# Kernel tuning notes

Measured on AMD Instinct MI355X. Metric: run time of the kernel, lower is better.

Reference implementation:

```python
import jax, jax.numpy as jnp
import numpy as np
from jax import lax

N, D, K = 8192, 1024, 80
M = 2048            # pre-NMS candidate budget (jit-static stand-in for nonzero())
TOPK = 100
IMG_H, IMG_W = 800.0, 1216.0
BW = (10.0, 10.0, 5.0, 5.0)            # Box2BoxTransform weights
SCALE_CLAMP = float(np.log(1000.0 / 16.0))
SCORE_T, NMS_T = 0.05, 0.5
MAX_COORD = max(IMG_H, IMG_W) + 1.0    # class offset for batched NMS


def setup_inputs() -> dict:
    key = jax.random.key(0)
    ks = jax.random.split(key, 5)
    x = jax.random.normal(ks[0], (N, D), jnp.float32)
    cls_w = jax.random.normal(ks[1], (D, K + 1), jnp.float32) * 0.1
    cls_b = jnp.zeros((K + 1,), jnp.float32)
    bbox_w = jax.random.normal(ks[2], (D, K * 4), jnp.float32) * 0.001
    bbox_b = jnp.zeros((K * 4,), jnp.float32)
    xy = jax.random.uniform(ks[3], (N, 2)) * jnp.array([IMG_W * 0.8, IMG_H * 0.8])
    wh = jax.random.uniform(ks[4], (N, 2)) * jnp.array([IMG_W * 0.2, IMG_H * 0.2]) + 8.0
    proposals = jnp.concatenate([xy, xy + wh], axis=1).astype(jnp.float32)  # [N,4] xyxy
    return {"x": x, "cls_w": cls_w, "cls_b": cls_b,
            "bbox_w": bbox_w, "bbox_b": bbox_b, "proposals": proposals}


def _apply_deltas(deltas, boxes):
    # deltas [N,K,4], boxes [N,4] xyxy -> decoded [N,K,4]
    w = boxes[:, 2] - boxes[:, 0]
    h = boxes[:, 3] - boxes[:, 1]
    cx = boxes[:, 0] + 0.5 * w
    cy = boxes[:, 1] + 0.5 * h
    dx = deltas[..., 0] / BW[0]
    dy = deltas[..., 1] / BW[1]
    dw = jnp.minimum(deltas[..., 2] / BW[2], SCALE_CLAMP)
    dh = jnp.minimum(deltas[..., 3] / BW[3], SCALE_CLAMP)
    pcx = dx * w[:, None] + cx[:, None]
    pcy = dy * h[:, None] + cy[:, None]
    pw = jnp.exp(dw) * w[:, None]
    ph = jnp.exp(dh) * h[:, None]
    return jnp.stack([pcx - 0.5 * pw, pcy - 0.5 * ph,
                      pcx + 0.5 * pw, pcy + 0.5 * ph], axis=-1)


def _clip(b):
    x1 = jnp.clip(b[..., 0], 0.0, IMG_W)
    y1 = jnp.clip(b[..., 1], 0.0, IMG_H)
    x2 = jnp.clip(b[..., 2], 0.0, IMG_W)
    y2 = jnp.clip(b[..., 3], 0.0, IMG_H)
    return jnp.stack([x1, y1, x2, y2], axis=-1)


def _pairwise_iou(b):  # [M,4] -> [M,M]
    x1 = jnp.maximum(b[:, None, 0], b[None, :, 0])
    y1 = jnp.maximum(b[:, None, 1], b[None, :, 1])
    x2 = jnp.minimum(b[:, None, 2], b[None, :, 2])
    y2 = jnp.minimum(b[:, None, 3], b[None, :, 3])
    inter = jnp.maximum(x2 - x1, 0.0) * jnp.maximum(y2 - y1, 0.0)
    area = (b[:, 2] - b[:, 0]) * (b[:, 3] - b[:, 1])
    union = area[:, None] + area[None, :] - inter
    return inter / jnp.maximum(union, 1e-9)


def _pipeline(x, cls_w, cls_b, bbox_w, bbox_b, proposals):
    probs = jax.nn.softmax(x @ cls_w + cls_b, axis=-1)[:, :K]   # drop bg col
    deltas = (x @ bbox_w + bbox_b).reshape(N, K, 4)
    boxes = _clip(_apply_deltas(deltas, proposals))             # [N,K,4]

    flat = probs.reshape(-1)                                    # [N*K]
    cand = jnp.where(flat > SCORE_T, flat, -1.0)
    top_scores, top_idx = lax.top_k(cand, M)                    # sorted desc
    prop_idx = top_idx // K
    cls_idx = top_idx % K
    cand_boxes = boxes[prop_idx, cls_idx]                       # [M,4]
    valid = top_scores > SCORE_T

    # batched NMS via per-class coordinate offsets
    off = cls_idx.astype(cand_boxes.dtype)[:, None] * MAX_COORD
    iou = _pairwise_iou(cand_boxes + off)
    idxs = jnp.arange(M)

    def body(i, sup):
        alive = jnp.logical_and(~sup[i], valid[i])
        return sup | (alive & (iou[i] > NMS_T) & (idxs > i))

    sup = lax.fori_loop(0, M, body, jnp.zeros((M,), bool))
    keep = valid & ~sup

    kept_scores = jnp.where(keep, top_scores, -1.0)
    fscores, fidx = lax.top_k(kept_scores, TOPK)
    fboxes = cand_boxes[fidx]
    fcls = cls_idx[fidx]
    fvalid = keep[fidx]
    return fboxes, fscores, fcls, fvalid


def reference(x, cls_w, cls_b, bbox_w, bbox_b, proposals):
    return _pipeline(x, cls_w, cls_b, bbox_w, bbox_b, proposals)
```

## Files before the change

### kernel.cpp

```cpp
#include <hip/hip_runtime.h>
#include <math.h>

typedef unsigned long long u64;
typedef unsigned int u32;

#define N_ROWS 8192
#define DIM 1024
#define KCLS 80
#define KC1 81
#define MCAND 2048
#define TOPK_ 100
#define CMAX 65536
#define ECAP 4096
#define ROWS_CAP 4096
#define EROWS 3
#define EKS 4
#define EKL (DIM / EKS)
#define FRPB 8
#define NSPLIT 16
#define NBINS 8192
#define BIN_BASE 125440
#define LCAP 1024
#define SCORE_T 0.05
#define NMS_T 0.5f
#define MAX_COORD_F 1217.0f
#define SCALE_CLAMP_F 4.135166556742356f
#define IMG_W_F 1216.0f
#define IMG_H_F 800.0f

#define GBM 32
#define GBK 64
#define PSTR 96
#define WFRAG (32 * 6 * 64 * 8)

typedef __attribute__((ext_vector_type(8))) short bf16x8;
typedef __attribute__((ext_vector_type(4))) float f32x4;

__device__ __forceinline__ int score_bin_f(float p) {
  u32 bits = __float_as_uint(p);
  int b = (int)(bits >> 13) - BIN_BASE;
  return b < 0 ? 0 : (b > NBINS - 1 ? NBINS - 1 : b);
}

__device__ __forceinline__ u64 readlane64(u64 v, int l) {
  u32 lo = __builtin_amdgcn_readlane((u32)v, l);
  u32 hi = __builtin_amdgcn_readlane((u32)(v >> 32), l);
  return ((u64)hi << 32) | (u64)lo;
}

__device__ __forceinline__ ushort f32_bf16(float f) {
  u32 b = __float_as_uint(f);
  b += 0x7FFFu + ((b >> 16) & 1u);
  return (ushort)(b >> 16);
}

__global__ __launch_bounds__(256) void k_prep(
    int* counter, int* ecount, int* rowcnt, int* hist, int* cnt,
    u32* rowflag, double* selS, u32* selI,
    const float4* __restrict__ bw4, float4* __restrict__ wT4,
    const float* __restrict__ w, ushort* __restrict__ whiF,
    ushort* __restrict__ wloF)
{
  int t = blockIdx.x * 256 + threadIdx.x;
  if (t == 0) { *counter = 0; *ecount = 0; *rowcnt = 0; }
  if (t < NBINS) hist[t] = 0;
  if (t < N_ROWS) rowflag[t] = 0;
  if (t < ECAP) cnt[t] = 0;
  if (t < MCAND) { selS[t] = -1.0; selI[t] = 0u; }
  if (t < KCLS * DIM) {
    int k = t / KCLS;
    int cls = t - k * KCLS;
    wT4[(size_t)cls * DIM + k] = bw4[t];
  }
  if (t < WFRAG) {
    int j = t & 7;
    int l = (t >> 3) & 63;
    int sf = t >> 9;
    int f = sf % 6;
    int s = sf / 6;
    int k = s * 32 + (l >> 4) * 8 + j;
    int c = f * 16 + (l & 15);
    float v = (c < KC1) ? w[(size_t)k * KC1 + c] : 0.0f;
    ushort hi = f32_bf16(v);
    float hf = __uint_as_float((u32)hi << 16);
    whiF[t] = hi;
    wloF[t] = f32_bf16(v - hf);
  }
}

__global__ __launch_bounds__(256) void k_gemm_sm(
    const float* __restrict__ x, const ushort* __restrict__ whiF,
    const ushort* __restrict__ wloF, const float* __restrict__ bias,
    float* __restrict__ scf, u32* __restrict__ cid,
    int* __restrict__ counter, int* __restrict__ hist)
{
  __shared__ __align__(16) char smem[33792];
  __shared__ float lgs[GBM * PSTR];
  __shared__ int lcnt, gbase;

  ushort (*xhi)[72] = (ushort(*)[72])(smem);
  ushort (*xlo)[72] = (ushort(*)[72])(smem + 4608);
  uint4* bhi = (uint4*)(smem + 9216);
  uint4* blo = (uint4*)(smem + 21504);
  u32* lhist = (u32*)(smem);
  float* lscf = (float*)(smem + 16384);
  u32* lcid = (u32*)(smem + 20480);
  float (*red)[32] = (float(*)[32])(smem + 24576);
  float* rowM = (float*)(smem + 26624);
  float* rowS = (float*)(smem + 26752);

  const int tid = threadIdx.x;
  const int rb = blockIdx.x * GBM;
  const int l = tid & 63;
  const int wv = tid >> 6;
  const int rh = wv & 1;
  const int ch = wv >> 1;

  if (tid == 0) lcnt = 0;

  f32x4 acc0 = {0.f, 0.f, 0.f, 0.f};
  f32x4 acc1 = {0.f, 0.f, 0.f, 0.f};
  f32x4 acc2 = {0.f, 0.f, 0.f, 0.f};

  const int srow = tid >> 3;
  const int skq = (tid & 7) * 8;
  const float* xsrc = x + (size_t)(rb + srow) * DIM + skq;

  const int ar = rh * 16 + (l & 15);
  const int ak = (l >> 4) * 8;
  const int bbase = (ch * 3) * 64 + l;

  for (int kt = 0; kt < DIM; kt += GBK) {
    float4 xv0 = *(const float4*)(xsrc + kt);
    float4 xv1 = *(const float4*)(xsrc + kt + 4);
    const uint4* bh = (const uint4*)whiF + (size_t)(kt >> 5) * 384;
    const uint4* bl = (const uint4*)wloF + (size_t)(kt >> 5) * 384;
    uint4 h0 = bh[tid], h1 = bh[tid + 256], h2 = bh[tid + 512];
    uint4 g0 = bl[tid], g1 = bl[tid + 256], g2 = bl[tid + 512];

    __syncthreads();

    {
      float vv[8] = {xv0.x, xv0.y, xv0.z, xv0.w, xv1.x, xv1.y, xv1.z, xv1.w};
      u32 hw[4], lw[4];
#pragma unroll
      for (int q = 0; q < 4; ++q) {
        ushort ha = f32_bf16(vv[2 * q]);
        ushort hb = f32_bf16(vv[2 * q + 1]);
        ushort la = f32_bf16(vv[2 * q] - __uint_as_float((u32)ha << 16));
        ushort lb = f32_bf16(vv[2 * q + 1] - __uint_as_float((u32)hb << 16));
        hw[q] = (u32)ha | ((u32)hb << 16);
        lw[q] = (u32)la | ((u32)lb << 16);
      }
      *(uint4*)&xhi[srow][skq] = make_uint4(hw[0], hw[1], hw[2], hw[3]);
      *(uint4*)&xlo[srow][skq] = make_uint4(lw[0], lw[1], lw[2], lw[3]);
      bhi[tid] = h0; bhi[tid + 256] = h1; bhi[tid + 512] = h2;
      blo[tid] = g0; blo[tid + 256] = g1; blo[tid + 512] = g2;
    }
    __syncthreads();

#pragma unroll
    for (int ks = 0; ks < 2; ++ks) {
      bf16x8 ah = *(const bf16x8*)&xhi[ar][ks * 32 + ak];
      bf16x8 al = *(const bf16x8*)&xlo[ar][ks * 32 + ak];
      bf16x8 b0h = *(const bf16x8*)&bhi[ks * 384 + bbase];
      bf16x8 b0l = *(const bf16x8*)&blo[ks * 384 + bbase];
      bf16x8 b1h = *(const bf16x8*)&bhi[ks * 384 + bbase + 64];
      bf16x8 b1l = *(const bf16x8*)&blo[ks * 384 + bbase + 64];
      bf16x8 b2h = *(const bf16x8*)&bhi[ks * 384 + bbase + 128];
      bf16x8 b2l = *(const bf16x8*)&blo[ks * 384 + bbase + 128];
      acc0 = __builtin_amdgcn_mfma_f32_16x16x32_bf16(ah, b0h, acc0, 0, 0, 0);
      acc0 = __builtin_amdgcn_mfma_f32_16x16x32_bf16(ah, b0l, acc0, 0, 0, 0);
      acc0 = __builtin_amdgcn_mfma_f32_16x16x32_bf16(al, b0h, acc0, 0, 0, 0);
      acc1 = __builtin_amdgcn_mfma_f32_16x16x32_bf16(ah, b1h, acc1, 0, 0, 0);
      acc1 = __builtin_amdgcn_mfma_f32_16x16x32_bf16(ah, b1l, acc1, 0, 0, 0);
      acc1 = __builtin_amdgcn_mfma_f32_16x16x32_bf16(al, b1h, acc1, 0, 0, 0);
      acc2 = __builtin_amdgcn_mfma_f32_16x16x32_bf16(ah, b2h, acc2, 0, 0, 0);
      acc2 = __builtin_amdgcn_mfma_f32_16x16x32_bf16(ah, b2l, acc2, 0, 0, 0);
      acc2 = __builtin_amdgcn_mfma_f32_16x16x32_bf16(al, b2h, acc2, 0, 0, 0);
    }
  }

  __syncthreads();
  {
    const int row0l = rh * 16 + (l >> 4) * 4;
    const int col0 = ch * 48 + (l & 15);
#pragma unroll
    for (int r = 0; r < 4; ++r) {
      lgs[(row0l + r) * PSTR + col0 + 0]  = acc0[r];
      lgs[(row0l + r) * PSTR + col0 + 16] = acc1[r];
      lgs[(row0l + r) * PSTR + col0 + 32] = acc2[r];
    }
  }
  for (int e = tid; e < NBINS / 2; e += 256) lhist[e] = 0u;
  __syncthreads();

  const int cx = tid >> 4;
  const int ry = tid & 15;
  float lg[2][6];
#pragma unroll
  for (int i = 0; i < 2; i++) {
    int rloc = ry * 2 + i;
#pragma unroll
    for (int j = 0; j < 6; j++) {
      int c = cx * 6 + j;
      lg[i][j] = (c < KC1) ? (lgs[rloc * PSTR + c] + bias[c]) : -1e30f;
    }
  }
  float pm[2] = {-1e30f, -1e30f};
#pragma unroll
  for (int i = 0; i < 2; i++)
#pragma unroll
    for (int j = 0; j < 6; j++) pm[i] = fmaxf(pm[i], lg[i][j]);
  red[cx][ry * 2 + 0] = pm[0];
  red[cx][ry * 2 + 1] = pm[1];
  __syncthreads();
  if (tid < 32) {
    float m = -1e30f;
#pragma unroll
    for (int q = 0; q < 16; q++) m = fmaxf(m, red[q][tid]);
    rowM[tid] = m;
  }
  __syncthreads();
  float ps[2] = {0.0f, 0.0f};
#pragma unroll
  for (int i = 0; i < 2; i++) {
    float m = rowM[ry * 2 + i];
#pragma unroll
    for (int j = 0; j < 6; j++) {
      int c = cx * 6 + j;
      if (c < KC1) ps[i] += expf(lg[i][j] - m);
    }
  }
  __syncthreads();
  red[cx][ry * 2 + 0] = ps[0];
  red[cx][ry * 2 + 1] = ps[1];
  __syncthreads();
  if (tid < 32) {
    float s = 0.0f;
#pragma unroll
    for (int q = 0; q < 16; q++) s += red[q][tid];
    rowS[tid] = s;
  }
  __syncthreads();
#pragma unroll
  for (int i = 0; i < 2; i++) {
    int rloc = ry * 2 + i;
    float m = rowM[rloc], s = rowS[rloc];
#pragma unroll
    for (int j = 0; j < 6; j++) {
      int c = cx * 6 + j;
      if (c < KCLS) {
        float p = expf(lg[i][j] - m) / s;
        if (p > 0.0485f) {
          int pos = atomicAdd(&lcnt, 1);
          u32 idx = (u32)((rb + rloc) * KCLS + c);
          if (pos < LCAP) { lscf[pos] = p; lcid[pos] = idx; }
          else {
            int g = atomicAdd(counter, 1);
            if (g < CMAX) { scf[g] = p; cid[g] = idx; }
          }
        }
        if (p > 0.051f) {
          int b = score_bin_f(p);
          atomicAdd(&lhist[b >> 1], 1u << ((b & 1) * 16));
        }
      }
    }
  }
  __syncthreads();
  if (tid == 0) {
    int n = min(lcnt, LCAP);
    gbase = atomicAdd(counter, n);
  }
  __syncthreads();
  {
    int n = min(lcnt, LCAP);
    for (int e = tid; e < n; e += 256) {
      int g = gbase + e;
      if (g < CMAX) { scf[g] = lscf[e]; cid[g] = lcid[e]; }
    }
  }
  for (int q = tid; q < NBINS / 2; q += 256) {
    u32 v = lhist[q];
    if (v) {
      u32 lo = v & 0xFFFFu, hi = v >> 16;
      if (lo) atomicAdd(&hist[q * 2 + 0], (int)lo);
      if (hi) atomicAdd(&hist[q * 2 + 1], (int)hi);
    }
  }
}

__global__ __launch_bounds__(256) void k_superset(
    const float* __restrict__ scf, const u32* __restrict__ cid,
    const int* __restrict__ counter, const int* __restrict__ hist,
    u32* __restrict__ elist, int* __restrict__ ecount, u32* __restrict__ rowflag)
{
  __shared__ int h[NBINS];
  __shared__ int segsum[256];
  __shared__ int segsuf[256];
  __shared__ int tbin_s;
  int C = *counter; if (C > CMAX) C = CMAX;
  if (blockIdx.x * 256 >= C) return;
  const int tid = threadIdx.x;
  if (tid == 0) tbin_s = 0;
  for (int e = tid; e < NBINS; e += 256) h[e] = hist[e];
  __syncthreads();
  {
    int s = 0;
#pragma unroll
    for (int q = 0; q < NBINS / 256; ++q) s += h[tid * (NBINS / 256) + q];
    segsum[tid] = s;
  }
  __syncthreads();
  if (tid == 0) {
    int run = 0;
    for (int t = 255; t >= 0; --t) { segsuf[t] = run; run += segsum[t]; }
  }
  __syncthreads();
  {
    int run = segsuf[tid];
    if (run < MCAND) {
      const int lo = tid * (NBINS / 256);
      for (int b = lo + NBINS / 256 - 1; b >= lo; --b) {
        run += h[b];
        if (run >= MCAND) { tbin_s = b; break; }
      }
    }
  }
  __syncthreads();
  int TM = tbin_s - 6; if (TM < 0) TM = 0;
  int e = blockIdx.x * 256 + tid;
  const int lane = tid & 63;
  bool pred = false;
  if (e < C) pred = (score_bin_f(scf[e]) >= TM);
  u64 m = __ballot(pred);
  if (m) {
    int leader = __ffsll((long long)m) - 1;
    int base = 0;
    if (lane == leader) base = atomicAdd(ecount, (int)__popcll(m));
    base = __shfl(base, leader);
    if (pred) {
      int j = base + (int)__popcll(m & ((lane == 63) ? ~0ull >> 1 : ((1ull << lane) - 1)));
      if (j < ECAP) {
        u32 idx = cid[e];
        elist[j] = idx;
        rowflag[idx / KCLS] = 1u;
      }
    }
  }
}

__global__ __launch_bounds__(256) void k_rowlist(
    const u32* __restrict__ rowflag, int* __restrict__ rowslot,
    u32* __restrict__ rowlist, int* __restrict__ rowcnt)
{
  int r = blockIdx.x * 256 + threadIdx.x;
  const int lane = threadIdx.x & 63;
  bool pred = (r < N_ROWS) && rowflag[r];
  u64 m = __ballot(pred);
  if (m) {
    int leader = __ffsll((long long)m) - 1;
    int base = 0;
    if (lane == leader) base = atomicAdd(rowcnt, (int)__popcll(m));
    base = __shfl(base, leader);
    if (pred) {
      int s = base + (int)__popcll(m & ((lane == 63) ? ~0ull >> 1 : ((1ull << lane) - 1)));
      if (s < ROWS_CAP) { rowslot[r] = s; rowlist[s] = (u32)r; }
    }
  }
}

__global__ __launch_bounds__(256) void k_exact_part(
    const u32* __restrict__ rowlist, const int* __restrict__ rowcnt,
    const float* __restrict__ x, const float* __restrict__ w,
    double* __restrict__ pexa)
{
  __shared__ double xt[EROWS][EKL];
  int rc = *rowcnt; if (rc > ROWS_CAP) rc = ROWS_CAP;
  const int rb = blockIdx.x * EROWS;
  if (rb >= rc) return;
  const int ks = blockIdx.y;
  const int kt0 = ks * EKL;
  const int tid = threadIdx.x;

  if (tid < EROWS * (EKL / 4)) {
    int srow = tid >> 6;
    int sf = tid & 63;
    int slot = rb + srow; if (slot >= rc) slot = rb;
    const float* xrow = x + (size_t)rowlist[slot] * DIM + kt0;
    float4 xv = *(const float4*)(xrow + sf * 4);
    xt[srow][sf * 4 + 0] = (double)xv.x;
    xt[srow][sf * 4 + 1] = (double)xv.y;
    xt[srow][sf * 4 + 2] = (double)xv.z;
    xt[srow][sf * 4 + 3] = (double)xv.w;
  }
  __syncthreads();

  const int row = tid / KC1;
  const int c = tid - row * KC1;
  if (row < EROWS && rb + row < rc) {
    const float* wp = w + (size_t)kt0 * KC1 + c;
    const double* xr = xt[row];
    double a = 0.0;
#pragma unroll 8
    for (int kk = 0; kk < EKL; ++kk) {
      a = fma(xr[kk], (double)wp[(size_t)kk * KC1], a);
    }
    pexa[((size_t)(rb + row) * EKS + ks) * KC1 + c] = a;
  }
}

__global__ __launch_bounds__(128) void k_exact_fin(
    const double* __restrict__ pexa, const int* __restrict__ rowcnt,
    const float* __restrict__ bias, double* __restrict__ prow)
{
  __shared__ double lg[FRPB][KC1];
  __shared__ double mv[FRPB], sv[FRPB];
  int rc = *rowcnt; if (rc > ROWS_CAP) rc = ROWS_CAP;
  const int rb = blockIdx.x * FRPB;
  if (rb >= rc) return;
  const int tid = threadIdx.x;
  const int nr = min(FRPB, rc - rb);

  if (tid < KC1) {
    for (int rr = 0; rr < nr; ++rr) {
      const double* pp = pexa + ((size_t)(rb + rr) * EKS) * KC1 + tid;
      double a = pp[0 * KC1];
      a += pp[1 * KC1];
      a += pp[2 * KC1];
      a += pp[3 * KC1];
      lg[rr][tid] = a + (double)bias[tid];
    }
  }
  __syncthreads();
  if (tid < nr) {
    double m = -1e300;
    for (int c2 = 0; c2 < KC1; ++c2) m = fmax(m, lg[tid][c2]);
    mv[tid] = m;
  }
  __syncthreads();
  if (tid < KC1) {
    for (int rr = 0; rr < nr; ++rr) lg[rr][tid] = exp(lg[rr][tid] - mv[rr]);
  }
  __syncthreads();
  if (tid < nr) {
    double s = 0.0;
    for (int c2 = 0; c2 < KC1; ++c2) s += lg[tid][c2];
    sv[tid] = s;
  }
  __syncthreads();
  if (tid < KC1) {
    for (int rr = 0; rr < nr; ++rr)
      prow[(size_t)(rb + rr) * KC1 + tid] = lg[rr][tid] / sv[rr];
  }
}

__global__ __launch_bounds__(256) void k_build(
    const u32* __restrict__ elist, const int* __restrict__ ecount,
    const int* __restrict__ rowslot, const double* __restrict__ prow,
    double* __restrict__ ssc, u32* __restrict__ sid)
{
  int E = *ecount; if (E > ECAP) E = ECAP;
  int e = blockIdx.x * 256 + threadIdx.x;
  if (e < E) {
    u32 idx = elist[e];
    int row = (int)(idx / KCLS);
    int cls = (int)(idx - (u32)row * KCLS);
    double p = prow[(size_t)rowslot[row] * KC1 + cls];
    ssc[e] = (p > SCORE_T) ? p : -1.0;
    sid[e] = idx;
  }
}

__global__ __launch_bounds__(256) void k_rank(
    const double* __restrict__ ssc, const u32* __restrict__ sid,
    const int* __restrict__ ecount, int* __restrict__ cnt)
{
  __shared__ double lsc[512];
  __shared__ u32 lid[512];
  int S = *ecount; if (S > ECAP) S = ECAP;
  const int i = blockIdx.x * 256 + threadIdx.x;
  if (blockIdx.x * 256 >= S) return;
  const double si = (i < S) ? ssc[i] : -2.0;
  const u32 ii = (i < S) ? sid[i] : 0u;
  const int seg = (S + NSPLIT - 1) / NSPLIT;
  const int jlo = blockIdx.y * seg;
  const int jhi = min(S, jlo + seg);
  int c = 0;
  for (int base = jlo; base < jhi; base += 512) {
    const int n = min(512, jhi - base);
    __syncthreads();
    for (int e = threadIdx.x; e < n; e += 256) { lsc[e] = ssc[base + e]; lid[e] = sid[base + e]; }
    __syncthreads();
    if (i < S) {
      int j = 0;
      for (; j + 8 <= n; j += 8) {
        double s0 = lsc[j + 0], s1 = lsc[j + 1], s2 = lsc[j + 2], s3 = lsc[j + 3];
        double s4 = lsc[j + 4], s5 = lsc[j + 5], s6 = lsc[j + 6], s7 = lsc[j + 7];
        u32 d0 = lid[j + 0], d1 = lid[j + 1], d2 = lid[j + 2], d3 = lid[j + 3];
        u32 d4 = lid[j + 4], d5 = lid[j + 5], d6 = lid[j + 6], d7 = lid[j + 7];
        c += (s0 > si || (s0 == si && d0 < ii)) ? 1 : 0;
        c += (s1 > si || (s1 == si && d1 < ii)) ? 1 : 0;
        c += (s2 > si || (s2 == si && d2 < ii)) ? 1 : 0;
        c += (s3 > si || (s3 == si && d3 < ii)) ? 1 : 0;
        c += (s4 > si || (s4 == si && d4 < ii)) ? 1 : 0;
        c += (s5 > si || (s5 == si && d5 < ii)) ? 1 : 0;
        c += (s6 > si || (s6 == si && d6 < ii)) ? 1 : 0;
        c += (s7 > si || (s7 == si && d7 < ii)) ? 1 : 0;
      }
      for (; j < n; ++j) {
        double sj = lsc[j];
        c += (sj > si || (sj == si && lid[j] < ii)) ? 1 : 0;
      }
    }
  }
  if (i < S && c > 0) atomicAdd(&cnt[i], c);
}

__global__ __launch_bounds__(256) void k_scatter(
    const double* __restrict__ ssc, const u32* __restrict__ sid,
    const int* __restrict__ ecount, const int* __restrict__ cnt,
    double* __restrict__ selS, u32* __restrict__ selI)
{
  int S = *ecount; if (S > ECAP) S = ECAP;
  const int i = blockIdx.x * 256 + threadIdx.x;
  if (i < S) {
    int c = cnt[i];
    if (c < MCAND) { selS[c] = ssc[i]; selI[c] = sid[i]; }
  }
}

__global__ __launch_bounds__(256) void k_gather_decode(
    const double* __restrict__ selS, const u32* __restrict__ selI,
    const float* __restrict__ x, const float4* __restrict__ wT4,
    const float* __restrict__ bbias, const float* __restrict__ proposals,
    float4* __restrict__ dbox, float4* __restrict__ obox,
    float* __restrict__ areav, float* __restrict__ scorev,
    int* __restrict__ clsv, int* __restrict__ validv)
{
  __shared__ double wred[4][4];
  const int r = blockIdx.x;
  const double s = selS[r];
  const u32 idx = selI[r];
  const int row = (int)(idx / 80u);
  const int cls = (int)(idx - (u32)row * 80u);

  const float* xr = x + (size_t)row * DIM;
  const float4* wc = wT4 + (size_t)cls * DIM;
  double a0 = 0, a1 = 0, a2 = 0, a3 = 0;
  for (int k = threadIdx.x; k < DIM; k += 256) {
    double xv = (double)xr[k];
    float4 wv = wc[k];
    a0 = fma(xv, (double)wv.x, a0);
    a1 = fma(xv, (double)wv.y, a1);
    a2 = fma(xv, (double)wv.z, a2);
    a3 = fma(xv, (double)wv.w, a3);
  }
#pragma unroll
  for (int off = 32; off > 0; off >>= 1) {
    a0 += __shfl_down(a0, off);
    a1 += __shfl_down(a1, off);
    a2 += __shfl_down(a2, off);
    a3 += __shfl_down(a3, off);
  }
  int lane = threadIdx.x & 63, wid = threadIdx.x >> 6;
  if (lane == 0) { wred[wid][0] = a0; wred[wid][1] = a1; wred[wid][2] = a2; wred[wid][3] = a3; }
  __syncthreads();
  if (threadIdx.x == 0) {
    double d0 = wred[0][0] + wred[1][0] + wred[2][0] + wred[3][0] + (double)bbias[cls * 4 + 0];
    double d1 = wred[0][1] + wred[1][1] + wred[2][1] + wred[3][1] + (double)bbias[cls * 4 + 1];
    double d2 = wred[0][2] + wred[1][2] + wred[2][2] + wred[3][2] + (double)bbias[cls * 4 + 2];
    double d3 = wred[0][3] + wred[1][3] + wred[2][3] + wred[3][3] + (double)bbias[cls * 4 + 3];
    float4 p = ((const float4*)proposals)[row];
    float w = p.z - p.x, h = p.w - p.y;
    float cxx = p.x + 0.5f * w, cyy = p.y + 0.5f * h;
    float dx = (float)d0 / 10.0f;
    float dy = (float)d1 / 10.0f;
    float dw = fminf((float)d2 / 5.0f, SCALE_CLAMP_F);
    float dh = fminf((float)d3 / 5.0f, SCALE_CLAMP_F);
    float pcx = dx * w + cxx, pcy = dy * h + cyy;
    float pw = expf(dw) * w, ph = expf(dh) * h;
    float x1 = pcx - 0.5f * pw, y1 = pcy - 0.5f * ph;
    float x2 = pcx + 0.5f * pw, y2 = pcy + 0.5f * ph;
    x1 = fminf(fmaxf(x1, 0.0f), IMG_W_F);
    x2 = fminf(fmaxf(x2, 0.0f), IMG_W_F);
    y1 = fminf(fmaxf(y1, 0.0f), IMG_H_F);
    y2 = fminf(fmaxf(y2, 0.0f), IMG_H_F);
    float4 db = {x1, y1, x2, y2};
    dbox[r] = db;
    float ofs = (float)cls * MAX_COORD_F;
    float4 ob = {x1 + ofs, y1 + ofs, x2 + ofs, y2 + ofs};
    obox[r] = ob;
    areav[r] = (ob.z - ob.x) * (ob.w - ob.y);
    scorev[r] = (float)s;
    clsv[r] = cls;
    validv[r] = (s > SCORE_T) ? 1 : 0;
  }
}

__global__ __launch_bounds__(256) void k_nms_mask(
    const float4* __restrict__ obox, const float* __restrict__ areav,
    u64* __restrict__ maskT)
{
  __shared__ float4 sb[MCAND];
  __shared__ float sa[MCAND];
  const int i = blockIdx.x;
  for (int e = threadIdx.x; e < MCAND; e += 256) { sb[e] = obox[e]; sa[e] = areav[e]; }
  __syncthreads();
  float4 bi = sb[i];
  float ai = sa[i];
  int lane = threadIdx.x & 63, wid = threadIdx.x >> 6;
#pragma unroll
  for (int it = 0; it < MCAND / 256; ++it) {
    int j = it * 256 + threadIdx.x;
    float4 bj = sb[j];
    float xx1 = fmaxf(bi.x, bj.x);
    float yy1 = fmaxf(bi.y, bj.y);
    float xx2 = fminf(bi.z, bj.z);
    float yy2 = fminf(bi.w, bj.w);
    float inter = fmaxf(xx2 - xx1, 0.0f) * fmaxf(yy2 - yy1, 0.0f);
    float uni = ai + sa[j] - inter;
    float iou = inter / fmaxf(uni, 1e-9f);
    bool pred = (iou > NMS_T) && (j > i);
    u64 b = __ballot(pred);
    if (lane == 0) maskT[(size_t)(it * 4 + wid) * MCAND + i] = b;
  }
}

__global__ __launch_bounds__(256) void k_nms_fin(
    const u64* __restrict__ maskT, const int* __restrict__ validv,
    const float4* __restrict__ dbox, const float* __restrict__ scorev,
    const int* __restrict__ clsv, float* __restrict__ out)
{
  __shared__ char ksh[MCAND];
  __shared__ short fidx[TOPK_];
  const int tid = threadIdx.x;

  if (tid < 64) {
    const int lane = tid;
    u64 validw = 0;
    for (int k = 0; k < 32; ++k) {
      u64 b = __ballot(validv[k * 64 + lane] != 0);
      validw = (lane == k) ? b : validw;
    }

    u64 alivew = 0;
    u64 supw = 0;
    int total = 0;
    int lastc = 31;

    for (int c = 0; c < 32; ++c) {
      const u64* col = maskT + (size_t)c * MCAND;
      u64 acc = 0;
      for (int t0 = 0; t0 < c; t0 += 8) {
        u64 r0 = 0, r1 = 0, r2 = 0, r3 = 0, r4 = 0, r5 = 0, r6 = 0, r7 = 0;
        if (t0 + 0 < c) r0 = col[(t0 + 0) * 64 + lane];
        if (t0 + 1 < c) r1 = col[(t0 + 1) * 64 + lane];
        if (t0 + 2 < c) r2 = col[(t0 + 2) * 64 + lane];
        if (t0 + 3 < c) r3 = col[(t0 + 3) * 64 + lane];
        if (t0 + 4 < c) r4 = col[(t0 + 4) * 64 + lane];
        if (t0 + 5 < c) r5 = col[(t0 + 5) * 64 + lane];
        if (t0 + 6 < c) r6 = col[(t0 + 6) * 64 + lane];
        if (t0 + 7 < c) r7 = col[(t0 + 7) * 64 + lane];
        u64 a;
        a = readlane64(alivew, t0 + 0); acc |= r0 & ((u64)0 - ((a >> lane) & 1ull));
        if (t0 + 1 < c) { a = readlane64(alivew, t0 + 1); acc |= r1 & ((u64)0 - ((a >> lane) & 1ull)); }
        if (t0 + 2 < c) { a = readlane64(alivew, t0 + 2); acc |= r2 & ((u64)0 - ((a >> lane) & 1ull)); }
        if (t0 + 3 < c) { a = readlane64(alivew, t0 + 3); acc |= r3 & ((u64)0 - ((a >> lane) & 1ull)); }
        if (t0 + 4 < c) { a = readlane64(alivew, t0 + 4); acc |= r4 & ((u64)0 - ((a >> lane) & 1ull)); }
        if (t0 + 5 < c) { a = readlane64(alivew, t0 + 5); acc |= r5 & ((u64)0 - ((a >> lane) & 1ull)); }
        if (t0 + 6 < c) { a = readlane64(alivew, t0 + 6); acc |= r6 & ((u64)0 - ((a >> lane) & 1ull)); }
        if (t0 + 7 < c) { a = readlane64(alivew, t0 + 7); acc |= r7 & ((u64)0 - ((a >> lane) & 1ull)); }
      }
      u64 d = col[(size_t)c * 64 + lane];
      acc |= (u64)__shfl_xor((long long)acc, 1);
      acc |= (u64)__shfl_xor((long long)acc, 2);
      acc |= (u64)__shfl_xor((long long)acc, 4);
      acc |= (u64)__shfl_xor((long long)acc, 8);
      acc |= (u64)__shfl_xor((long long)acc, 16);
      acc |= (u64)__shfl_xor((long long)acc, 32);
      u64 s_sup = acc;
      u64 s_val = readlane64(validw, c);
      u64 aliveM = 0;
#pragma unroll
      for (int b = 0; b < 64; ++b) {
        u32 rhi = __builtin_amdgcn_readlane((u32)(d >> 32), b);
        u32 rlo = (b < 31) ? __builtin_amdgcn_readlane((u32)d, b) : 0u;
        u64 row = ((u64)rhi << 32) | (u64)rlo;
        u64 act = ((s_val >> b) & 1ull) & (~(s_sup >> b) & 1ull);
        s_sup |= row & ((u64)0 - act);
        aliveM |= act << b;
      }
      alivew = (lane == c) ? aliveM : alivew;
      supw   = (lane == c) ? s_sup  : supw;
      total += (int)__popcll(aliveM);
      if (total >= TOPK_) { lastc = c; break; }
    }

    for (int k = 0; k < 32; ++k) {
      int e = k * 64 + lane;
      if (k <= lastc) {
        u64 s = readlane64(supw, k);
        int sb = (int)((s >> lane) & 1ull);
        ksh[e] = (char)((validv[e] && !sb) ? 1 : 0);
      } else {
        ksh[e] = 0;
      }
    }
  }
  __syncthreads();
  if (tid == 0) {
    int cnt = 0;
    for (int r = 0; r < MCAND && cnt < TOPK_; ++r) if (ksh[r]) fidx[cnt++] = (short)r;
    for (int r = 0; r < MCAND && cnt < TOPK_; ++r) if (!ksh[r]) fidx[cnt++] = (short)r;
  }
  __syncthreads();
  if (tid < TOPK_) {
    int r = fidx[tid];
    float4 b = dbox[r];
    out[tid * 4 + 0] = b.x; out[tid * 4 + 1] = b.y;
    out[tid * 4 + 2] = b.z; out[tid * 4 + 3] = b.w;
    int kp = ksh[r];
    out[400 + tid] = kp ? scorev[r] : -1.0f;
    out[500 + tid] = (float)clsv[r];
    out[600 + tid] = kp ? 1.0f : 0.0f;
  }
}

extern "C" void kernel_launch(void* const* d_in, const int* in_sizes, int n_in,
                              void* d_out, int out_size, void* d_ws, size_t ws_size,
                              hipStream_t stream) {
  const float* x         = (const float*)d_in[0];
  const float* cls_w     = (const float*)d_in[1];
  const float* cls_b     = (const float*)d_in[2];
  const float* bbox_w    = (const float*)d_in[3];
  const float* bbox_b    = (const float*)d_in[4];
  const float* proposals = (const float*)d_in[5];
  float* out = (float*)d_out;

  char* ws = (char*)d_ws;
  size_t off = 0;
  float*  part  = (float*)(ws + off);  off += (size_t)4 * N_ROWS * KC1 * 4;
  float4* wT4   = (float4*)(ws + off); off += (size_t)KCLS * DIM * 16;
  ushort* whiF  = (ushort*)(ws + off); off += (size_t)WFRAG * 2;
  ushort* wloF  = (ushort*)(ws + off); off += (size_t)WFRAG * 2;
  float*  scf   = (float*)(ws + off);  off += (size_t)CMAX * 4;
  u32*    cid   = (u32*)(ws + off);    off += (size_t)CMAX * 4;
  int*    hist  = (int*)(ws + off);    off += (size_t)NBINS * 4;
  u32*    rowflag = (u32*)(ws + off);  off += (size_t)N_ROWS * 4;
  int*    rowslot = (int*)(ws + off);  off += (size_t)N_ROWS * 4;
  u32*    rowlist = (u32*)(ws + off);  off += (size_t)ROWS_CAP * 4;
  u32*    elist = (u32*)(ws + off);    off += (size_t)ECAP * 4;
  double* prow  = (double*)(ws + off); off += (size_t)ROWS_CAP * KC1 * 8;
  double* ssc   = (double*)(ws + off); off += (size_t)ECAP * 8;
  u32*    sid   = (u32*)(ws + off);    off += (size_t)ECAP * 4;
  int*    cnt   = (int*)(ws + off);    off += (size_t)ECAP * 4;
  double* selS  = (double*)(ws + off); off += (size_t)MCAND * 8;
  u32*    selI  = (u32*)(ws + off);    off += (size_t)MCAND * 4;
  off = (off + 15) & ~(size_t)15;
  int*    counter = (int*)(ws + off);  off += 16;
  int*    ecount  = (int*)(ws + off);  off += 16;
  int*    rowcnt  = (int*)(ws + off);  off += 16;
  float4* dbox  = (float4*)(ws + off); off += (size_t)MCAND * 16;
  float4* obox  = (float4*)(ws + off); off += (size_t)MCAND * 16;
  float*  areav = (float*)(ws + off);  off += (size_t)MCAND * 4;
  float*  scorev= (float*)(ws + off);  off += (size_t)MCAND * 4;
  int*    clsv  = (int*)(ws + off);    off += (size_t)MCAND * 4;
  int*    validv= (int*)(ws + off);    off += (size_t)MCAND * 4;
  off = (off + 15) & ~(size_t)15;
  u64*    maskT = (u64*)(ws + off);    off += (size_t)MCAND * 32 * 8;

  double* pexa = (double*)part;

  k_prep<<<WFRAG / 256, 256, 0, stream>>>(counter, ecount, rowcnt, hist, cnt,
                                          rowflag, selS, selI,
                                          (const float4*)bbox_w, wT4,
                                          cls_w, whiF, wloF);
  k_gemm_sm<<<N_ROWS / GBM, 256, 0, stream>>>(x, whiF, wloF, cls_b,
                                              scf, cid, counter, hist);
  k_superset<<<CMAX / 256, 256, 0, stream>>>(scf, cid, counter, hist,
                                             elist, ecount, rowflag);
  k_rowlist<<<N_ROWS / 256, 256, 0, stream>>>(rowflag, rowslot, rowlist, rowcnt);
  k_exact_part<<<dim3((ROWS_CAP + EROWS - 1) / EROWS, EKS), 256, 0, stream>>>(
      rowlist, rowcnt, x, cls_w, pexa);
  k_exact_fin<<<ROWS_CAP / FRPB, 128, 0, stream>>>(pexa, rowcnt, cls_b, prow);
  k_build<<<ECAP / 256, 256, 0, stream>>>(elist, ecount, rowslot, prow, ssc, sid);
  k_rank<<<dim3(ECAP / 256, NSPLIT), 256, 0, stream>>>(ssc, sid, ecount, cnt);
  k_scatter<<<ECAP / 256, 256, 0, stream>>>(ssc, sid, ecount, cnt, selS, selI);
  k_gather_decode<<<MCAND, 256, 0, stream>>>(selS, selI, x, wT4, bbox_b, proposals,
                                             dbox, obox, areav, scorev, clsv, validv);
  k_nms_mask<<<MCAND, 256, 0, stream>>>(obox, areav, maskT);
  k_nms_fin<<<1, 256, 0, stream>>>(maskT, validv, dbox, scorev, clsv, out);
}
```

Before: 211.8 us.

## Fuse split-K exact logits and softmax into one kernel per row group

Merges the split-K double-precision logit kernel and the separate softmax-finalize kernel into a single kernel. Each block now covers the full K dimension with four independent accumulators, then does the max and sum reductions in shared memory and writes the probabilities directly. This removes one launch and the global round-trip of partial sums, but each block does four times the serial work and the grid has four times fewer blocks. It also stages the valid flags in shared memory inside the NMS finish kernel instead of reading them twice from global memory.

Measured after the change: 215.6 us. No clear change (+1.8%).

```diff
diff --git a/kernel.cpp b/kernel.cpp
--- a/kernel.cpp
+++ b/kernel.cpp
@@ -14,9 +14,6 @@
 #define ECAP 4096
 #define ROWS_CAP 4096
 #define EROWS 3
-#define EKS 4
-#define EKL (DIM / EKS)
-#define FRPB 8
 #define NSPLIT 16
 #define NBINS 8192
 #define BIN_BASE 125440
@@ -371,88 +368,74 @@
   }
 }
 
-__global__ __launch_bounds__(256) void k_exact_part(
+__global__ __launch_bounds__(256) void k_exact(
     const u32* __restrict__ rowlist, const int* __restrict__ rowcnt,
     const float* __restrict__ x, const float* __restrict__ w,
-    double* __restrict__ pexa)
-{
-  __shared__ double xt[EROWS][EKL];
+    const float* __restrict__ bias, double* __restrict__ prow)
+{
+  __shared__ double xt[EROWS][DIM];
+  __shared__ double red[EROWS][128];
   int rc = *rowcnt; if (rc > ROWS_CAP) rc = ROWS_CAP;
   const int rb = blockIdx.x * EROWS;
   if (rb >= rc) return;
-  const int ks = blockIdx.y;
-  const int kt0 = ks * EKL;
   const int tid = threadIdx.x;
 
-  if (tid < EROWS * (EKL / 4)) {
-    int srow = tid >> 6;
-    int sf = tid & 63;
+  for (int q = tid; q < EROWS * (DIM / 4); q += 256) {
+    int srow = q >> 8;
+    int sf = q & 255;
     int slot = rb + srow; if (slot >= rc) slot = rb;
-    const float* xrow = x + (size_t)rowlist[slot] * DIM + kt0;
+    const float* xrow = x + (size_t)rowlist[slot] * DIM;
     float4 xv = *(const float4*)(xrow + sf * 4);
     xt[srow][sf * 4 + 0] = (double)xv.x;
     xt[srow][sf * 4 + 1] = (double)xv.y;
     xt[srow][sf * 4 + 2] = (double)xv.z;
     xt[srow][sf * 4 + 3] = (double)xv.w;
   }
+  for (int q = tid; q < EROWS * 128; q += 256) ((double*)red)[q] = -1e300;
   __syncthreads();
 
   const int row = tid / KC1;
   const int c = tid - row * KC1;
-  if (row < EROWS && rb + row < rc) {
-    const float* wp = w + (size_t)kt0 * KC1 + c;
+  const bool act = (row < EROWS);
+  double a = 0.0;
+  if (act) {
     const double* xr = xt[row];
-    double a = 0.0;
+    double a0 = 0.0, a1 = 0.0, a2 = 0.0, a3 = 0.0;
 #pragma unroll 8
-    for (int kk = 0; kk < EKL; ++kk) {
-      a = fma(xr[kk], (double)wp[(size_t)kk * KC1], a);
-    }
-    pexa[((size_t)(rb + row) * EKS + ks) * KC1 + c] = a;
-  }
-}
-
-__global__ __launch_bounds__(128) void k_exact_fin(
-    const double* __restrict__ pexa, const int* __restrict__ rowcnt,
-    const float* __restrict__ bias, double* __restrict__ prow)
-{
-  __shared__ double lg[FRPB][KC1];
-  __shared__ double mv[FRPB], sv[FRPB];
-  int rc = *rowcnt; if (rc > ROWS_CAP) rc = ROWS_CAP;
-  const int rb = blockIdx.x * FRPB;
-  if (rb >= rc) return;
-  const int tid = threadIdx.x;
-  const int nr = min(FRPB, rc - rb);
-
-  if (tid < KC1) {
-    for (int rr = 0; rr < nr; ++rr) {
-      const double* pp = pexa + ((size_t)(rb + rr) * EKS) * KC1 + tid;
-      double a = pp[0 * KC1];
-      a += pp[1 * KC1];
-      a += pp[2 * KC1];
-      a += pp[3 * KC1];
-      lg[rr][tid] = a + (double)bias[tid];
-    }
-  }
-  __syncthreads();
-  if (tid < nr) {
-    double m = -1e300;
-    for (int c2 = 0; c2 < KC1; ++c2) m = fmax(m, lg[tid][c2]);
-    mv[tid] = m;
-  }
-  __syncthreads();
-  if (tid < KC1) {
-    for (int rr = 0; rr < nr; ++rr) lg[rr][tid] = exp(lg[rr][tid] - mv[rr]);
-  }
-  __syncthreads();
-  if (tid < nr) {
-    double s = 0.0;
-    for (int c2 = 0; c2 < KC1; ++c2) s += lg[tid][c2];
-    sv[tid] = s;
-  }
-  __syncthreads();
-  if (tid < KC1) {
-    for (int rr = 0; rr < nr; ++rr)
-      prow[(size_t)(rb + rr) * KC1 + tid] = lg[rr][tid] / sv[rr];
+    for (int kk = 0; kk < DIM / 4; ++kk) {
+      a0 = fma(xr[kk          ], (double)w[(size_t)(kk          ) * KC1 + c], a0);
+      a1 = fma(xr[kk + 256    ], (double)w[(size_t)(kk + 256    ) * KC1 + c], a1);
+      a2 = fma(xr[kk + 512    ], (double)w[(size_t)(kk + 512    ) * KC1 + c], a2);
+      a3 = fma(xr[kk + 768    ], (double)w[(size_t)(kk + 768    ) * KC1 + c], a3);
+    }
+    a = a0 + a1 + a2 + a3 + (double)bias[c];
+    red[row][c] = a;
+  }
+  __syncthreads();
+  if (act && c < 64) { double o = red[row][c + 64]; if (o > red[row][c]) red[row][c] = o; }
+  __syncthreads();
+#pragma unroll
+  for (int off = 32; off > 0; off >>= 1) {
+    if (act && c < off) { double o = red[row][c + off]; if (o > red[row][c]) red[row][c] = o; }
+    __syncthreads();
+  }
+  double m = act ? red[row][0] : 0.0;
+  __syncthreads();
+  double e = act ? exp(a - m) : 0.0;
+  for (int q = tid; q < EROWS * 128; q += 256) ((double*)red)[q] = 0.0;
+  __syncthreads();
+  if (act) red[row][c] = e;
+  __syncthreads();
+  if (act && c < 64) red[row][c] += red[row][c + 64];
+  __syncthreads();
+#pragma unroll
+  for (int off = 32; off > 0; off >>= 1) {
+    if (act && c < off) red[row][c] += red[row][c + off];
+    __syncthreads();
+  }
+  if (act && rb + row < rc) {
+    double s = red[row][0];
+    prow[(size_t)(rb + row) * KC1 + c] = e / s;
   }
 }
 
@@ -633,15 +616,19 @@
     const float4* __restrict__ dbox, const float* __restrict__ scorev,
     const int* __restrict__ clsv, float* __restrict__ out)
 {
+  __shared__ int vsh[MCAND];
   __shared__ char ksh[MCAND];
   __shared__ short fidx[TOPK_];
   const int tid = threadIdx.x;
+
+  for (int e = tid; e < MCAND; e += 256) vsh[e] = validv[e];
+  __syncthreads();
 
   if (tid < 64) {
     const int lane = tid;
     u64 validw = 0;
     for (int k = 0; k < 32; ++k) {
-      u64 b = __ballot(validv[k * 64 + lane] != 0);
+      u64 b = __ballot(vsh[k * 64 + lane] != 0);
       validw = (lane == k) ? b : validw;
     }
 
@@ -703,7 +690,7 @@
       if (k <= lastc) {
         u64 s = readlane64(supw, k);
         int sb = (int)((s >> lane) & 1ull);
-        ksh[e] = (char)((validv[e] && !sb) ? 1 : 0);
+        ksh[e] = (char)((vsh[e] && !sb) ? 1 : 0);
       } else {
         ksh[e] = 0;
       }
@@ -741,7 +728,6 @@
 
   char* ws = (char*)d_ws;
   size_t off = 0;
-  float*  part  = (float*)(ws + off);  off += (size_t)4 * N_ROWS * KC1 * 4;
   float4* wT4   = (float4*)(ws + off); off += (size_t)KCLS * DIM * 16;
   ushort* whiF  = (ushort*)(ws + off); off += (size_t)WFRAG * 2;
   ushort* wloF  = (ushort*)(ws + off); off += (size_t)WFRAG * 2;
@@ -771,8 +757,6 @@
   off = (off + 15) & ~(size_t)15;
   u64*    maskT = (u64*)(ws + off);    off += (size_t)MCAND * 32 * 8;
 
-  double* pexa = (double*)part;
-
   k_prep<<<WFRAG / 256, 256, 0, stream>>>(counter, ecount, rowcnt, hist, cnt,
                                           rowflag, selS, selI,
                                           (const float4*)bbox_w, wT4,
@@ -782,9 +766,8 @@
   k_superset<<<CMAX / 256, 256, 0, stream>>>(scf, cid, counter, hist,
                                              elist, ecount, rowflag);
   k_rowlist<<<N_ROWS / 256, 256, 0, stream>>>(rowflag, rowslot, rowlist, rowcnt);
-  k_exact_part<<<dim3((ROWS_CAP + EROWS - 1) / EROWS, EKS), 256, 0, stream>>>(
-      rowlist, rowcnt, x, cls_w, pexa);
-  k_exact_fin<<<ROWS_CAP / FRPB, 128, 0, stream>>>(pexa, rowcnt, cls_b, prow);
+  k_exact<<<(ROWS_CAP + EROWS - 1) / EROWS, 256, 0, stream>>>(
+      rowlist, rowcnt, x, cls_w, cls_b, prow);
   k_build<<<ECAP / 256, 256, 0, stream>>>(elist, ecount, rowslot, prow, ssc, sid);
   k_rank<<<dim3(ECAP / 256, NSPLIT), 256, 0, stream>>>(ssc, sid, ecount, cnt);
   k_scatter<<<ECAP / 256, 256, 0, stream>>>(ssc, sid, ecount, cnt, selS, selI);
```
